# Kernel tuning notes

Measured on AMD Instinct MI355X. Metric: run time of the kernel, lower is better.

The kernel has to match this reference:

```python
import jax, jax.numpy as jnp
import numpy as np

N = 4096; E = 131072
NUM_USERS = 50000; NUM_ITEMS = 41476
EMB = 64; HID1 = 1024; HID2 = 512; D = 256
NUM_CLASSES = 41476; EPS = 1e-5

def _seg(x, idx, n):
    return jax.ops.segment_sum(x, idx, num_segments=n)

def setup_inputs():
    key = jax.random.key(0)
    keys = iter(jax.random.split(key, 64))
    def nrm(shape, s=0.02):
        return jax.random.normal(next(keys), shape, jnp.float32) * s
    inp = {}
    inp['user_indices'] = jax.random.randint(next(keys), (N,), 0, NUM_USERS)
    inp['item_indices'] = jax.random.randint(next(keys), (N,), 0, NUM_ITEMS)
    inp['edge_index'] = jax.random.randint(next(keys), (2, E), 0, N)
    inp['emb_user'] = nrm((NUM_USERS, EMB), 1.0)
    inp['emb_item'] = nrm((NUM_ITEMS, EMB), 1.0)
    inp['mlp_w1'] = nrm((2 * EMB, HID1)); inp['mlp_b1'] = jnp.zeros((HID1,), jnp.float32)
    inp['mlp_w2'] = nrm((HID1, HID2)); inp['mlp_b2'] = jnp.zeros((HID2,), jnp.float32)
    inp['gcn_w0'] = nrm((HID2, D)); inp['gcn_b0'] = jnp.zeros((D,), jnp.float32)
    inp['bn_g0'] = jnp.ones((D,), jnp.float32); inp['bn_b0'] = jnp.zeros((D,), jnp.float32)
    inp['gcn_w1'] = nrm((D, D)); inp['gcn_b1'] = jnp.zeros((D,), jnp.float32)
    inp['bn_g1'] = jnp.ones((D,), jnp.float32); inp['bn_b1'] = jnp.zeros((D,), jnp.float32)
    inp['sage_wl'] = nrm((D, D)); inp['sage_bl'] = jnp.zeros((D,), jnp.float32); inp['sage_wr'] = nrm((D, D))
    inp['cheb_w0'] = nrm((D, D)); inp['cheb_w1'] = nrm((D, D)); inp['cheb_b'] = jnp.zeros((D,), jnp.float32)
    for h in range(2):
        inp[f'gat_w{h}'] = nrm((D, D)); inp[f'gat_asrc{h}'] = nrm((D,)); inp[f'gat_adst{h}'] = nrm((D,)); inp[f'gat_b{h}'] = jnp.zeros((D,), jnp.float32)
    inp['pred_w'] = nrm((D, NUM_CLASSES)); inp['pred_b'] = jnp.zeros((NUM_CLASSES,), jnp.float32)
    return inp

def _forward(user_indices, item_indices, edge_index, emb_user, emb_item, mlp_w1, mlp_b1, mlp_w2, mlp_b2, gcn_w0, gcn_b0, bn_g0, bn_b0, gcn_w1, gcn_b1, bn_g1, bn_b1, sage_wl, sage_bl, sage_wr, cheb_w0, cheb_w1, cheb_b, gat_w0, gat_asrc0, gat_adst0, gat_b0, gat_w1, gat_asrc1, gat_adst1, gat_b1, pred_w, pred_b):
    n = user_indices.shape[0]
    src, dst = edge_index[0], edge_index[1]
    # embedding lookup + concat + MLP (Dropout is identity at eval)
    x = jnp.concatenate([emb_user[user_indices], emb_item[item_indices]], axis=1)  # [n, 2*EMB]
    x = jax.nn.relu(x @ mlp_w1 + mlp_b1)
    x = jax.nn.relu(x @ mlp_w2 + mlp_b2)
    ones = jnp.ones((src.shape[0],), x.dtype)
    # GCNConv: symmetric norm with self loops, aggregate src -> dst
    deg = _seg(ones, dst, n) + 1.0
    dinv = deg ** -0.5
    coef = (dinv[src] * dinv[dst])[:, None]
    self_coef = (dinv * dinv)[:, None]
    for W, b, g, bt in ((gcn_w0, gcn_b0, bn_g0, bn_b0), (gcn_w1, gcn_b1, bn_g1, bn_b1)):
        xw = x @ W
        agg = _seg(xw[src] * coef, dst, n) + xw * self_coef + b
        mu = jnp.mean(agg, 0); var = jnp.var(agg, 0)  # BatchNorm1d, batch stats
        x = jax.nn.relu(g * (agg - mu) * jax.lax.rsqrt(var + EPS) + bt)
    # SAGEConv (mean aggregation): W_l * mean_nbr + b_l + W_r * x
    cnt = _seg(ones, dst, n)
    mean_nbr = _seg(x[src], dst, n) / jnp.maximum(cnt, 1.0)[:, None]
    x = jax.nn.relu(mean_nbr @ sage_wl + sage_bl + x @ sage_wr)
    dinv_c = jnp.where(cnt > 0, cnt ** -0.5, 0.0)
    tx1 = _seg(x[src] * (-(dinv_c[src] * dinv_c[dst]))[:, None], dst, n)
    x = jax.nn.relu(x @ cheb_w0 + tx1 @ cheb_w1 + cheb_b)
    # GATConv (heads=1, concat=False), self loops added
    loop = jnp.arange(n)
    src2 = jnp.concatenate([src, loop]); dst2 = jnp.concatenate([dst, loop])
    for W, a_s, a_d, b in ((gat_w0, gat_asrc0, gat_adst0, gat_b0), (gat_w1, gat_asrc1, gat_adst1, gat_b1)):
        xw = x @ W
        e = jax.nn.leaky_relu((xw @ a_s)[src2] + (xw @ a_d)[dst2], 0.2)
        m = jax.ops.segment_max(e, dst2, num_segments=n)
        ex = jnp.exp(e - m[dst2])
        alpha = (ex / _seg(ex, dst2, n)[dst2])[:, None]
        x = jax.nn.elu(_seg(xw[src2] * alpha, dst2, n) + b)
    return x @ pred_w + pred_b

def reference(user_indices, item_indices, edge_index, emb_user, emb_item, mlp_w1, mlp_b1, mlp_w2, mlp_b2, gcn_w0, gcn_b0, bn_g0, bn_b0, gcn_w1, gcn_b1, bn_g1, bn_b1, sage_wl, sage_bl, sage_wr, cheb_w0, cheb_w1, cheb_b, gat_w0, gat_asrc0, gat_adst0, gat_b0, gat_w1, gat_asrc1, gat_adst1, gat_b1, pred_w, pred_b):
    return _forward(user_indices, item_indices, edge_index, emb_user, emb_item, mlp_w1, mlp_b1, mlp_w2, mlp_b2, gcn_w0, gcn_b0, bn_g0, bn_b0, gcn_w1, gcn_b1, bn_g1, bn_b1, sage_wl, sage_bl, sage_wr, cheb_w0, cheb_w1, cheb_b, gat_w0, gat_asrc0, gat_adst0, gat_b0, gat_w1, gat_asrc1, gat_adst1, gat_b1, pred_w, pred_b)
```

## Files before the change

kernel.cpp:

```cpp
#include <hip/hip_runtime.h>
#include <hip/hip_bf16.h>
#include <math.h>

#define DIM 256
#define EMB 64
#define HID1 1024
#define HID2 512
#define EPSBN 1e-5f

typedef float f32x4 __attribute__((ext_vector_type(4)));
typedef __bf16 bf16x8 __attribute__((ext_vector_type(8)));

__device__ __forceinline__ unsigned short f2bf(float f) {
    unsigned u = __float_as_uint(f);
    unsigned r = (u + 0x7fffu + ((u >> 16) & 1u)) >> 16;
    return (unsigned short)r;
}
__device__ __forceinline__ float bf2f(unsigned short h) {
    return __uint_as_float(((unsigned)h) << 16);
}


__global__ __launch_bounds__(128) void k_embed(const int* __restrict__ ui, const int* __restrict__ ii,
                                               const float* __restrict__ eu, const float* __restrict__ ei,
                                               float* __restrict__ x0) {
    int i = blockIdx.x, t = threadIdx.x;
    float v = (t < 64) ? eu[(size_t)ui[i] * 64 + t] : ei[(size_t)ii[i] * 64 + (t - 64)];
    x0[(size_t)i * 128 + t] = v;
}

__global__ __launch_bounds__(256) void k_hist(const int* __restrict__ dst, int* __restrict__ cnt, int E) {
    int e = blockIdx.x * 256 + threadIdx.x;
    if (e < E) atomicAdd(&cnt[dst[e]], 1);
}

__global__ __launch_bounds__(1024) void k_scan4096(const int* __restrict__ cnt, int* __restrict__ roff) {
    __shared__ int s[1024];
    int t = threadIdx.x;
    int v0 = cnt[4*t], v1 = cnt[4*t+1], v2 = cnt[4*t+2], v3 = cnt[4*t+3];
    int loc = v0 + v1 + v2 + v3;
    s[t] = loc;
    for (int o = 1; o < 1024; o <<= 1) {
        __syncthreads();
        int x = (t >= o) ? s[t - o] : 0;
        __syncthreads();
        s[t] += x;
    }
    __syncthreads();
    int excl = s[t] - loc;
    roff[4*t]   = excl;
    roff[4*t+1] = excl + v0;
    roff[4*t+2] = excl + v0 + v1;
    roff[4*t+3] = excl + v0 + v1 + v2;
    if (t == 1023) roff[4096] = s[1023];
}

__global__ __launch_bounds__(256) void k_csr_fill(const int* __restrict__ src, const int* __restrict__ dst,
                                                  const int* __restrict__ roff, int* __restrict__ cursor,
                                                  int* __restrict__ csrc, int E) {
    int e = blockIdx.x * 256 + threadIdx.x;
    if (e < E) {
        int d = dst[e];
        int pos = roff[d] + atomicAdd(&cursor[d], 1);
        csrc[pos] = src[e];
    }
}

__global__ __launch_bounds__(256) void k_coefs(const int* __restrict__ cnt, float* __restrict__ dinv,
                                               float* __restrict__ dinvc, float* __restrict__ invc, int n) {
    int i = blockIdx.x * 256 + threadIdx.x;
    if (i < n) {
        int c = cnt[i];
        dinv[i]  = rsqrtf((float)c + 1.0f);
        dinvc[i] = (c > 0) ? rsqrtf((float)c) : 0.0f;
        invc[i]  = 1.0f / (float)(c > 0 ? c : 1);
    }
}

template<int BIAS, int RELU, int ACC>
__global__ __launch_bounds__(256) void gemm64(const float* __restrict__ A, const float* __restrict__ B,
                                              const float* __restrict__ bias, float* __restrict__ C,
                                              int M, int K, int N) {
    __shared__ float As[32][68];
    __shared__ float Bs[32][68];
    const int bn = blockIdx.x * 64, bm = blockIdx.y * 64;
    const int tid = threadIdx.x;
    const int tx = tid & 15, ty = tid >> 4;
    const int alm = tid >> 2;
    const int alk = (tid & 3) * 8;
    const int blk = tid >> 3;
    const int bln = (tid & 7) * 8;
    const bool nfull = (bn + 64 <= N);

    float acc[4][4] = {};

    for (int k0 = 0; k0 < K; k0 += 32) {
        const float* ap = A + (size_t)(bm + alm) * K + k0 + alk;
        float4 a0 = *(const float4*)ap;
        float4 a1 = *(const float4*)(ap + 4);
        As[alk+0][alm] = a0.x; As[alk+1][alm] = a0.y; As[alk+2][alm] = a0.z; As[alk+3][alm] = a0.w;
        As[alk+4][alm] = a1.x; As[alk+5][alm] = a1.y; As[alk+6][alm] = a1.z; As[alk+7][alm] = a1.w;

        const float* bp = B + (size_t)(k0 + blk) * N + bn + bln;
        if (nfull) {
            *(float4*)&Bs[blk][bln]     = *(const float4*)bp;
            *(float4*)&Bs[blk][bln + 4] = *(const float4*)(bp + 4);
        } else {
            #pragma unroll
            for (int j = 0; j < 8; ++j)
                Bs[blk][bln + j] = (bn + bln + j < N) ? bp[j] : 0.0f;
        }
        __syncthreads();
        #pragma unroll
        for (int k = 0; k < 32; ++k) {
            float4 av = *(const float4*)&As[k][ty * 4];
            float4 bv = *(const float4*)&Bs[k][tx * 4];
            float a[4] = {av.x, av.y, av.z, av.w};
            float b[4] = {bv.x, bv.y, bv.z, bv.w};
            #pragma unroll
            for (int i = 0; i < 4; ++i)
                #pragma unroll
                for (int j = 0; j < 4; ++j)
                    acc[i][j] = fmaf(a[i], b[j], acc[i][j]);
        }
        __syncthreads();
    }

    const int row = bm + ty * 4, col = bn + tx * 4;
    #pragma unroll
    for (int i = 0; i < 4; ++i) {
        float* cp = C + (size_t)(row + i) * N + col;
        #pragma unroll
        for (int j = 0; j < 4; ++j) {
            if (col + j < N) {
                float v = acc[i][j];
                if (ACC)  v += cp[j];
                if (BIAS) v += bias[col + j];
                if (RELU) v = fmaxf(v, 0.0f);
                cp[j] = v;
            }
        }
    }
}


__global__ __launch_bounds__(256) void k_convA(const float* __restrict__ X, unsigned short* __restrict__ Ah,
                                               unsigned short* __restrict__ Al, int total) {
    int i = blockIdx.x * 256 + threadIdx.x;
    if (i < total) {
        float f = X[i];
        unsigned short h = f2bf(f);
        Ah[i] = h;
        Al[i] = f2bf(f - bf2f(h));
    }
}

__global__ __launch_bounds__(256) void k_convB(const float* __restrict__ W, unsigned short* __restrict__ Bh,
                                               unsigned short* __restrict__ Bl, int K, int NC) {
    __shared__ float tile[64][65];
    const int n0 = blockIdx.x * 64, k0 = blockIdx.y * 64;
    const int t = threadIdx.x;
    const int tn = t & 63, tk4 = t >> 6;
    for (int kk = tk4; kk < 64; kk += 4) {
        int n = n0 + tn;
        tile[kk][tn] = (n < NC) ? W[(size_t)(k0 + kk) * NC + n] : 0.0f;
    }
    __syncthreads();
    const int wn = t >> 2, wk = (t & 3) * 16;
    size_t base = (size_t)(n0 + wn) * K + k0 + wk;
    #pragma unroll
    for (int j = 0; j < 16; ++j) {
        float f = tile[wk + j][wn];
        unsigned short h = f2bf(f);
        Bh[base + j] = h;
        Bl[base + j] = f2bf(f - bf2f(h));
    }
}

__global__ __launch_bounds__(256) void gemm_pred_mfma(
    const unsigned short* __restrict__ Ah, const unsigned short* __restrict__ Al,
    const unsigned short* __restrict__ Bh, const unsigned short* __restrict__ Bl,
    const float* __restrict__ bias, float* __restrict__ C, int NC) {
    __shared__ bf16x8 smem[2048];
    char* AsB = (char*)smem;
    char* BsB = (char*)smem + 16384;
    const int tid = threadIdx.x;
    const int w = tid >> 6, l = tid & 63;
    const int wr = w >> 1, wc = w & 1;
    const int g = l >> 4, lr = l & 15;
    const int bm = blockIdx.y * 128, bn = blockIdx.x * 128;

    f32x4 acc[4][4] = {};

    for (int t = 0; t < 12; ++t) {
        const int kk = (t & 3) * 64;
        const unsigned short* Ag = (t < 8) ? Ah : Al;
        const unsigned short* Bg = (t >= 4 && t < 8) ? Bl : Bh;
        #pragma unroll
        for (int c = 0; c < 4; ++c) {
            const int row = w * 32 + c * 8 + (l >> 3);
            const int q = l & 7;
            const int gs = q ^ (row & 7);
            const unsigned short* ga = Ag + (size_t)(bm + row) * 256 + kk + gs * 8;
            const unsigned short* gb = Bg + (size_t)(bn + row) * 256 + kk + gs * 8;
            __builtin_amdgcn_global_load_lds(
                (const __attribute__((address_space(1))) void*)ga,
                (__attribute__((address_space(3))) void*)(AsB + (w * 32 + c * 8) * 128), 16, 0, 0);
            __builtin_amdgcn_global_load_lds(
                (const __attribute__((address_space(1))) void*)gb,
                (__attribute__((address_space(3))) void*)(BsB + (w * 32 + c * 8) * 128), 16, 0, 0);
        }
        __syncthreads();
        #pragma unroll
        for (int ks = 0; ks < 2; ++ks) {
            bf16x8 af[4], bfr[4];
            #pragma unroll
            for (int m = 0; m < 4; ++m) {
                const int row = wr * 64 + m * 16 + lr;
                const int slot = (ks * 4 + g) ^ (row & 7);
                af[m] = *(const bf16x8*)(AsB + row * 128 + slot * 16);
            }
            #pragma unroll
            for (int n = 0; n < 4; ++n) {
                const int row = wc * 64 + n * 16 + lr;
                const int slot = (ks * 4 + g) ^ (row & 7);
                bfr[n] = *(const bf16x8*)(BsB + row * 128 + slot * 16);
            }
            #pragma unroll
            for (int m = 0; m < 4; ++m)
                #pragma unroll
                for (int n = 0; n < 4; ++n)
                    acc[m][n] = __builtin_amdgcn_mfma_f32_16x16x32_bf16(af[m], bfr[n], acc[m][n], 0, 0, 0);
        }
        __syncthreads();
    }
    #pragma unroll
    for (int n = 0; n < 4; ++n) {
        const int col = bn + wc * 64 + n * 16 + lr;
        if (col < NC) {
            const float bv = bias[col];
            #pragma unroll
            for (int m = 0; m < 4; ++m) {
                const int row0 = bm + wr * 64 + m * 16 + g * 4;
                #pragma unroll
                for (int r = 0; r < 4; ++r)
                    C[(size_t)(row0 + r) * NC + col] = acc[m][n][r] + bv;
            }
        }
    }
}


__global__ __launch_bounds__(256) void k_gcn_agg(const float* __restrict__ xw, const int* __restrict__ roff,
                                                 const int* __restrict__ csrc, const float* __restrict__ dinv,
                                                 const float* __restrict__ b, float* __restrict__ out) {
    int i = blockIdx.x, c = threadIdx.x;
    float di = dinv[i];
    float acc = xw[(size_t)i * DIM + c] * di * di;
    int beg = roff[i], end = roff[i + 1];
    for (int j = beg; j < end; ++j) {
        int s = csrc[j];
        acc = fmaf(xw[(size_t)s * DIM + c], dinv[s] * di, acc);
    }
    out[(size_t)i * DIM + c] = acc + b[c];
}

__global__ __launch_bounds__(256) void k_sage_agg(const float* __restrict__ x, const int* __restrict__ roff,
                                                  const int* __restrict__ csrc, const float* __restrict__ invc,
                                                  float* __restrict__ out) {
    int i = blockIdx.x, c = threadIdx.x;
    float acc = 0.0f;
    int beg = roff[i], end = roff[i + 1];
    for (int j = beg; j < end; ++j) acc += x[(size_t)csrc[j] * DIM + c];
    out[(size_t)i * DIM + c] = acc * invc[i];
}

__global__ __launch_bounds__(256) void k_cheb_agg(const float* __restrict__ x, const int* __restrict__ roff,
                                                  const int* __restrict__ csrc, const float* __restrict__ dinvc,
                                                  float* __restrict__ out) {
    int i = blockIdx.x, c = threadIdx.x;
    float dci = dinvc[i];
    float acc = 0.0f;
    int beg = roff[i], end = roff[i + 1];
    for (int j = beg; j < end; ++j) {
        int s = csrc[j];
        acc = fmaf(x[(size_t)s * DIM + c], -(dinvc[s] * dci), acc);
    }
    out[(size_t)i * DIM + c] = acc;
}


__global__ __launch_bounds__(256) void k_colstats(const float* __restrict__ X, float* __restrict__ sum,
                                                  float* __restrict__ sq) {
    int c = threadIdx.x;
    int r0 = blockIdx.x * 64;
    float s = 0.0f, q = 0.0f;
    for (int r = r0; r < r0 + 64; ++r) {
        float v = X[(size_t)r * DIM + c];
        s += v;
        q = fmaf(v, v, q);
    }
    atomicAdd(&sum[c], s);
    atomicAdd(&sq[c], q);
}

__global__ __launch_bounds__(256) void k_bnfin(const float* __restrict__ sum, const float* __restrict__ sq,
                                               float* __restrict__ mu, float* __restrict__ rstd, float invn) {
    int c = threadIdx.x;
    float m = sum[c] * invn;
    float var = sq[c] * invn - m * m;
    mu[c] = m;
    rstd[c] = rsqrtf(var + EPSBN);
}

__global__ __launch_bounds__(256) void k_bnapply(const float* __restrict__ X, const float* __restrict__ mu,
                                                 const float* __restrict__ rstd, const float* __restrict__ g,
                                                 const float* __restrict__ bt, float* __restrict__ out) {
    int r = blockIdx.x, c = threadIdx.x;
    size_t idx = (size_t)r * DIM + c;
    float v = (X[idx] - mu[c]) * rstd[c] * g[c] + bt[c];
    out[idx] = fmaxf(v, 0.0f);
}


__global__ __launch_bounds__(256) void k_gat_proj(const float* __restrict__ xw, const float* __restrict__ a_s,
                                                  const float* __restrict__ a_d, float* __restrict__ ps,
                                                  float* __restrict__ pd) {
    int i = blockIdx.x, t = threadIdx.x;
    __shared__ float r1[256], r2[256];
    float v = xw[(size_t)i * DIM + t];
    r1[t] = v * a_s[t];
    r2[t] = v * a_d[t];
    __syncthreads();
    for (int o = 128; o > 0; o >>= 1) {
        if (t < o) { r1[t] += r1[t + o]; r2[t] += r2[t + o]; }
        __syncthreads();
    }
    if (t == 0) { ps[i] = r1[0]; pd[i] = r2[0]; }
}

__device__ __forceinline__ float leaky02(float x) { return x > 0.0f ? x : 0.2f * x; }

__global__ __launch_bounds__(256) void k_gat_agg(const float* __restrict__ xw, const float* __restrict__ ps,
                                                 const float* __restrict__ pd, const int* __restrict__ roff,
                                                 const int* __restrict__ csrc, const float* __restrict__ b,
                                                 float* __restrict__ out) {
    int i = blockIdx.x, t = threadIdx.x;
    int beg = roff[i], end = roff[i + 1];
    float ad = pd[i];
    __shared__ float red[256];
    float lm = -1e30f;
    for (int j = beg + t; j < end; j += 256) lm = fmaxf(lm, leaky02(ps[csrc[j]] + ad));
    if (t == 0) lm = fmaxf(lm, leaky02(ps[i] + ad));
    red[t] = lm; __syncthreads();
    for (int o = 128; o > 0; o >>= 1) { if (t < o) red[t] = fmaxf(red[t], red[t + o]); __syncthreads(); }
    float m = red[0]; __syncthreads();
    float ls = 0.0f;
    for (int j = beg + t; j < end; j += 256) ls += __expf(leaky02(ps[csrc[j]] + ad) - m);
    if (t == 0) ls += __expf(leaky02(ps[i] + ad) - m);
    red[t] = ls; __syncthreads();
    for (int o = 128; o > 0; o >>= 1) { if (t < o) red[t] += red[t + o]; __syncthreads(); }
    float inv_s = 1.0f / red[0];
    float acc = __expf(leaky02(ps[i] + ad) - m) * xw[(size_t)i * DIM + t];
    for (int j = beg; j < end; ++j) {
        int s = csrc[j];
        acc = fmaf(__expf(leaky02(ps[s] + ad) - m), xw[(size_t)s * DIM + t], acc);
    }
    float v = acc * inv_s + b[t];
    out[(size_t)i * DIM + t] = v > 0.0f ? v : expm1f(v);
}


extern "C" void kernel_launch(void* const* d_in, const int* in_sizes, int n_in,
                              void* d_out, int out_size, void* d_ws, size_t ws_size,
                              hipStream_t stream) {
    const int*   ui  = (const int*)d_in[0];
    const int*   ii  = (const int*)d_in[1];
    const int*   edg = (const int*)d_in[2];
    const float* eu  = (const float*)d_in[3];
    const float* ei  = (const float*)d_in[4];
    const float* w1  = (const float*)d_in[5];  const float* b1  = (const float*)d_in[6];
    const float* w2  = (const float*)d_in[7];  const float* b2  = (const float*)d_in[8];
    const float* gw0 = (const float*)d_in[9];  const float* gb0 = (const float*)d_in[10];
    const float* bg0 = (const float*)d_in[11]; const float* bb0 = (const float*)d_in[12];
    const float* gw1 = (const float*)d_in[13]; const float* gb1 = (const float*)d_in[14];
    const float* bg1 = (const float*)d_in[15]; const float* bb1 = (const float*)d_in[16];
    const float* swl = (const float*)d_in[17]; const float* sbl = (const float*)d_in[18];
    const float* swr = (const float*)d_in[19];
    const float* cw0 = (const float*)d_in[20]; const float* cw1 = (const float*)d_in[21];
    const float* cb  = (const float*)d_in[22];
    const float* aw0 = (const float*)d_in[23]; const float* as0 = (const float*)d_in[24];
    const float* ad0 = (const float*)d_in[25]; const float* ab0 = (const float*)d_in[26];
    const float* aw1 = (const float*)d_in[27]; const float* as1 = (const float*)d_in[28];
    const float* ad1 = (const float*)d_in[29]; const float* ab1 = (const float*)d_in[30];
    const float* pw  = (const float*)d_in[31]; const float* pb  = (const float*)d_in[32];
    float* out = (float*)d_out;

    const int N  = in_sizes[0];
    const int E  = in_sizes[2] / 2;
    const int NC = in_sizes[32];
    const int NPAD = ((NC + 127) / 128) * 128;
    const int* src = edg;
    const int* dst = edg + E;

    char* p = (char*)d_ws;
    auto alloc = [&](size_t bytes) -> void* {
        void* r = (void*)p;
        p += ((bytes + 255) / 256) * 256;
        return r;
    };
    float* x0   = (float*)alloc((size_t)N * 128 * 4);
    float* h1   = (float*)alloc((size_t)N * HID1 * 4);
    float* h2   = (float*)alloc((size_t)N * HID2 * 4);
    float* xa   = (float*)alloc((size_t)N * DIM * 4);
    float* xb   = (float*)alloc((size_t)N * DIM * 4);
    float* xc   = (float*)alloc((size_t)N * DIM * 4);
    float* xd   = (float*)alloc((size_t)N * DIM * 4);
    float* dinv = (float*)alloc(N * 4);
    float* dinvc= (float*)alloc(N * 4);
    float* invc = (float*)alloc(N * 4);
    float* psrc = (float*)alloc(N * 4);
    float* pdst = (float*)alloc(N * 4);
    float* csum = (float*)alloc(256 * 4);
    float* csq  = (float*)alloc(256 * 4);
    float* mu   = (float*)alloc(256 * 4);
    float* rstd = (float*)alloc(256 * 4);
    int* cnt    = (int*)alloc(N * 4);
    int* cursor = (int*)alloc(N * 4);
    int* roff   = (int*)alloc((N + 1) * 4);
    int* csrc   = (int*)alloc((size_t)E * 4);
    unsigned short* Ah = (unsigned short*)alloc((size_t)N * DIM * 2);
    unsigned short* Al = (unsigned short*)alloc((size_t)N * DIM * 2);
    unsigned short* Bh = (unsigned short*)alloc((size_t)NPAD * DIM * 2);
    unsigned short* Bl = (unsigned short*)alloc((size_t)NPAD * DIM * 2);

    const int EB = (E + 255) / 256;
    dim3 blk256(256);

    hipMemsetAsync(cnt, 0, (size_t)N * 4, stream);
    hipMemsetAsync(cursor, 0, (size_t)N * 4, stream);
    k_hist<<<EB, blk256, 0, stream>>>(dst, cnt, E);
    k_scan4096<<<1, 1024, 0, stream>>>(cnt, roff);
    k_csr_fill<<<EB, blk256, 0, stream>>>(src, dst, roff, cursor, csrc, E);
    k_coefs<<<(N + 255) / 256, blk256, 0, stream>>>(cnt, dinv, dinvc, invc, N);

    k_convB<<<dim3(NPAD / 64, DIM / 64), blk256, 0, stream>>>(pw, Bh, Bl, DIM, NC);

    k_embed<<<N, 128, 0, stream>>>(ui, ii, eu, ei, x0);
    gemm64<1,1,0><<<dim3(HID1/64, N/64), blk256, 0, stream>>>(x0, w1, b1, h1, N, 128, HID1);
    gemm64<1,1,0><<<dim3(HID2/64, N/64), blk256, 0, stream>>>(h1, w2, b2, h2, N, HID1, HID2);

    gemm64<0,0,0><<<dim3(DIM/64, N/64), blk256, 0, stream>>>(h2, gw0, nullptr, xb, N, HID2, DIM);
    k_gcn_agg<<<N, blk256, 0, stream>>>(xb, roff, csrc, dinv, gb0, xc);
    hipMemsetAsync(csum, 0, 256 * 4, stream);
    hipMemsetAsync(csq, 0, 256 * 4, stream);
    k_colstats<<<N / 64, blk256, 0, stream>>>(xc, csum, csq);
    k_bnfin<<<1, 256, 0, stream>>>(csum, csq, mu, rstd, 1.0f / (float)N);
    k_bnapply<<<N, blk256, 0, stream>>>(xc, mu, rstd, bg0, bb0, xa);

    gemm64<0,0,0><<<dim3(DIM/64, N/64), blk256, 0, stream>>>(xa, gw1, nullptr, xb, N, DIM, DIM);
    k_gcn_agg<<<N, blk256, 0, stream>>>(xb, roff, csrc, dinv, gb1, xc);
    hipMemsetAsync(csum, 0, 256 * 4, stream);
    hipMemsetAsync(csq, 0, 256 * 4, stream);
    k_colstats<<<N / 64, blk256, 0, stream>>>(xc, csum, csq);
    k_bnfin<<<1, 256, 0, stream>>>(csum, csq, mu, rstd, 1.0f / (float)N);
    k_bnapply<<<N, blk256, 0, stream>>>(xc, mu, rstd, bg1, bb1, xa);

    k_sage_agg<<<N, blk256, 0, stream>>>(xa, roff, csrc, invc, xd);
    gemm64<0,0,0><<<dim3(DIM/64, N/64), blk256, 0, stream>>>(xa, swr, nullptr, xb, N, DIM, DIM);
    gemm64<1,1,1><<<dim3(DIM/64, N/64), blk256, 0, stream>>>(xd, swl, sbl, xb, N, DIM, DIM);

    k_cheb_agg<<<N, blk256, 0, stream>>>(xb, roff, csrc, dinvc, xd);
    gemm64<0,0,0><<<dim3(DIM/64, N/64), blk256, 0, stream>>>(xb, cw0, nullptr, xc, N, DIM, DIM);
    gemm64<1,1,1><<<dim3(DIM/64, N/64), blk256, 0, stream>>>(xd, cw1, cb, xc, N, DIM, DIM);

    gemm64<0,0,0><<<dim3(DIM/64, N/64), blk256, 0, stream>>>(xc, aw0, nullptr, xb, N, DIM, DIM);
    k_gat_proj<<<N, blk256, 0, stream>>>(xb, as0, ad0, psrc, pdst);
    k_gat_agg<<<N, blk256, 0, stream>>>(xb, psrc, pdst, roff, csrc, ab0, xa);

    gemm64<0,0,0><<<dim3(DIM/64, N/64), blk256, 0, stream>>>(xa, aw1, nullptr, xb, N, DIM, DIM);
    k_gat_proj<<<N, blk256, 0, stream>>>(xb, as1, ad1, psrc, pdst);
    k_gat_agg<<<N, blk256, 0, stream>>>(xb, psrc, pdst, roff, csrc, ab1, xc);

    k_convA<<<(N * DIM + 255) / 256, blk256, 0, stream>>>(xc, Ah, Al, N * DIM);
    gemm_pred_mfma<<<dim3(NPAD / 128, N / 128), blk256, 0, stream>>>(Ah, Al, Bh, Bl, pb, out, NC);
}
```

Measured before the change: 1.626 ms.

## Load all bf16 split parts per K-step and swap grid order in pred GEMM

The split-bf16 prediction GEMM now stages the high and low parts of A and B together for each 64-wide K slice and issues all three MFMA products per fragment in one pass. The old version ran 12 separate K passes that reloaded the same tiles. This cuts the number of barriers and redundant global-to-LDS loads. LDS use grows to 64KB per block, which may reduce occupancy, and the grid is transposed so that consecutive blocks walk along M and share the same B column tile for L2 reuse.

```diff
diff --git a/kernel.cpp b/kernel.cpp
--- a/kernel.cpp
+++ b/kernel.cpp
@@ -181,56 +181,67 @@
     const unsigned short* __restrict__ Ah, const unsigned short* __restrict__ Al,
     const unsigned short* __restrict__ Bh, const unsigned short* __restrict__ Bl,
     const float* __restrict__ bias, float* __restrict__ C, int NC) {
-    __shared__ bf16x8 smem[2048];
-    char* AsB = (char*)smem;
-    char* BsB = (char*)smem + 16384;
+    __shared__ char lds[65536];
+    char* AhS = lds;
+    char* AlS = lds + 16384;
+    char* BhS = lds + 32768;
+    char* BlS = lds + 49152;
     const int tid = threadIdx.x;
     const int w = tid >> 6, l = tid & 63;
     const int wr = w >> 1, wc = w & 1;
     const int g = l >> 4, lr = l & 15;
-    const int bm = blockIdx.y * 128, bn = blockIdx.x * 128;
+    const int bm = blockIdx.x * 128, bn = blockIdx.y * 128;
 
     f32x4 acc[4][4] = {};
 
-    for (int t = 0; t < 12; ++t) {
-        const int kk = (t & 3) * 64;
-        const unsigned short* Ag = (t < 8) ? Ah : Al;
-        const unsigned short* Bg = (t >= 4 && t < 8) ? Bl : Bh;
+    for (int kk = 0; kk < 256; kk += 64) {
         #pragma unroll
         for (int c = 0; c < 4; ++c) {
             const int row = w * 32 + c * 8 + (l >> 3);
             const int q = l & 7;
             const int gs = q ^ (row & 7);
-            const unsigned short* ga = Ag + (size_t)(bm + row) * 256 + kk + gs * 8;
-            const unsigned short* gb = Bg + (size_t)(bn + row) * 256 + kk + gs * 8;
+            const size_t goffA = (size_t)(bm + row) * 256 + kk + gs * 8;
+            const size_t goffB = (size_t)(bn + row) * 256 + kk + gs * 8;
+            const int ldsoff = (w * 32 + c * 8) * 128;
             __builtin_amdgcn_global_load_lds(
-                (const __attribute__((address_space(1))) void*)ga,
-                (__attribute__((address_space(3))) void*)(AsB + (w * 32 + c * 8) * 128), 16, 0, 0);
+                (const __attribute__((address_space(1))) void*)(Ah + goffA),
+                (__attribute__((address_space(3))) void*)(AhS + ldsoff), 16, 0, 0);
             __builtin_amdgcn_global_load_lds(
-                (const __attribute__((address_space(1))) void*)gb,
-                (__attribute__((address_space(3))) void*)(BsB + (w * 32 + c * 8) * 128), 16, 0, 0);
+                (const __attribute__((address_space(1))) void*)(Al + goffA),
+                (__attribute__((address_space(3))) void*)(AlS + ldsoff), 16, 0, 0);
+            __builtin_amdgcn_global_load_lds(
+                (const __attribute__((address_space(1))) void*)(Bh + goffB),
+                (__attribute__((address_space(3))) void*)(BhS + ldsoff), 16, 0, 0);
+            __builtin_amdgcn_global_load_lds(
+                (const __attribute__((address_space(1))) void*)(Bl + goffB),
+                (__attribute__((address_space(3))) void*)(BlS + ldsoff), 16, 0, 0);
         }
         __syncthreads();
         #pragma unroll
         for (int ks = 0; ks < 2; ++ks) {
-            bf16x8 af[4], bfr[4];
+            bf16x8 ah[4], al[4], bh[4], bl[4];
             #pragma unroll
             for (int m = 0; m < 4; ++m) {
                 const int row = wr * 64 + m * 16 + lr;
                 const int slot = (ks * 4 + g) ^ (row & 7);
-                af[m] = *(const bf16x8*)(AsB + row * 128 + slot * 16);
+                ah[m] = *(const bf16x8*)(AhS + row * 128 + slot * 16);
+                al[m] = *(const bf16x8*)(AlS + row * 128 + slot * 16);
             }
             #pragma unroll
             for (int n = 0; n < 4; ++n) {
                 const int row = wc * 64 + n * 16 + lr;
                 const int slot = (ks * 4 + g) ^ (row & 7);
-                bfr[n] = *(const bf16x8*)(BsB + row * 128 + slot * 16);
+                bh[n] = *(const bf16x8*)(BhS + row * 128 + slot * 16);
+                bl[n] = *(const bf16x8*)(BlS + row * 128 + slot * 16);
             }
             #pragma unroll
             for (int m = 0; m < 4; ++m)
                 #pragma unroll
-                for (int n = 0; n < 4; ++n)
-                    acc[m][n] = __builtin_amdgcn_mfma_f32_16x16x32_bf16(af[m], bfr[n], acc[m][n], 0, 0, 0);
+                for (int n = 0; n < 4; ++n) {
+                    acc[m][n] = __builtin_amdgcn_mfma_f32_16x16x32_bf16(ah[m], bh[n], acc[m][n], 0, 0, 0);
+                    acc[m][n] = __builtin_amdgcn_mfma_f32_16x16x32_bf16(ah[m], bl[n], acc[m][n], 0, 0, 0);
+                    acc[m][n] = __builtin_amdgcn_mfma_f32_16x16x32_bf16(al[m], bh[n], acc[m][n], 0, 0, 0);
+                }
         }
         __syncthreads();
     }
@@ -483,5 +494,5 @@
     k_gat_agg<<<N, blk256, 0, stream>>>(xb, psrc, pdst, roff, csrc, ab1, xc);
 
     k_convA<<<(N * DIM + 255) / 256, blk256, 0, stream>>>(xc, Ah, Al, N * DIM);
-    gemm_pred_mfma<<<dim3(NPAD / 128, N / 128), blk256, 0, stream>>>(Ah, Al, Bh, Bl, pb, out, NC);
-}
+    gemm_pred_mfma<<<dim3(N / 128, NPAD / 128), blk256, 0, stream>>>(Ah, Al, Bh, Bl, pb, out, NC);
+}
```

Result: faster. 1.587 ms (-2.4%).
